# Kernel tuning notes

Measured on AMD Instinct MI355X. Metric: run time of the kernel, lower is better.

Reference implementation:

```python
import jax, jax.numpy as jnp
import numpy as np

N_NODES = 100_000
E_TOTAL = 1_100_000
# up_scale_edge_ranges: static metadata on the Data object -> baked as constants
EXCLUDE_RANGES = [(1_000_000, 1_100_000)]
_mask = np.ones(E_TOTAL, dtype=bool)
for _s, _e in EXCLUDE_RANGES:
    _mask[_s:_e] = False
KEEP_IDX = np.nonzero(_mask)[0]  # static, shape [1_000_000]


def _mlp(h, w1, b1, w2, b2):
    return jax.nn.relu(h @ w1 + b1) @ w2 + b2


def setup_inputs() -> dict:
    key = jax.random.key(0)
    ks = jax.random.split(key, 12)
    s = 0.05
    return {
        "x": jax.random.normal(ks[0], (N_NODES, 7), dtype=jnp.float32),
        "pos": jax.random.normal(ks[1], (N_NODES, 3), dtype=jnp.float32),
        "edge_index": jax.random.randint(ks[2], (2, E_TOTAL), 0, N_NODES, dtype=jnp.int64),
        "nw1": jax.random.normal(ks[3], (7, 128), dtype=jnp.float32) * s,
        "nb1": jnp.zeros((128,), dtype=jnp.float32),
        "nw2": jax.random.normal(ks[4], (128, 128), dtype=jnp.float32) * s,
        "nb2": jnp.zeros((128,), dtype=jnp.float32),
        "ew1": jax.random.normal(ks[5], (3, 128), dtype=jnp.float32) * s,
        "eb1": jnp.zeros((128,), dtype=jnp.float32),
        "ew2": jax.random.normal(ks[6], (128, 128), dtype=jnp.float32) * s,
        "eb2": jnp.zeros((128,), dtype=jnp.float32),
    }


def reference(x, pos, edge_index, nw1, nb1, nw2, nb2, ew1, eb1, ew2, eb2):
    # static mask over edge ranges (shapes fixed at trace time)
    edges = edge_index[:, KEEP_IDX]                       # [2, E_kept]
    d = pos[edges[0], :2] - pos[edges[1], :2]             # [E_kept, 2]
    norm = jnp.linalg.norm(d, axis=1, keepdims=True)      # [E_kept, 1]
    edges_attr = jnp.concatenate([d, norm], axis=1)       # [E_kept, 3]
    edge_embedding = _mlp(edges_attr, ew1, eb1, ew2, eb2) # [E_kept, 128]
    node_embedding = _mlp(x, nw1, nb1, nw2, nb2)          # [N, 128]
    return (node_embedding, edge_embedding)
```

## Files before the change

kernel.cpp:

```cpp
#include <hip/hip_runtime.h>

typedef short short8 __attribute__((ext_vector_type(8)));
typedef float f32x4 __attribute__((ext_vector_type(4)));
typedef unsigned int u32x2 __attribute__((ext_vector_type(2)));
typedef unsigned int u32x4 __attribute__((ext_vector_type(4)));

#define N_NODES   100000
#define E_KEEP    1000000
#define E_TOTAL_N 1100000
#define EDGE_OUT_BASE 12800000L

#define H1_STRIDE 272
#define STG_STRIDE 272

__device__ __forceinline__ unsigned short f2bf(float f) {
  unsigned int u = __builtin_bit_cast(unsigned int, f);
  u += 0x7fffu + ((u >> 16) & 1u);
  return (unsigned short)(u >> 16);
}

__device__ __forceinline__ unsigned int cvtpk(float lo, float hi) {
  unsigned int r;
  asm("v_cvt_pk_bf16_f32 %0, %1, %2" : "=v"(r) : "v"(lo), "v"(hi));
  return r;
}
__device__ __forceinline__ unsigned int pack2relu(float lo, float hi) {
  return cvtpk(fmaxf(lo, 0.f), fmaxf(hi, 0.f));
}
__device__ __forceinline__ unsigned int pack2(float lo, float hi) {
  return cvtpk(lo, hi);
}

__global__ void transpose_w2(const float* __restrict__ nw2,
                             const float* __restrict__ ew2,
                             unsigned short* __restrict__ ws) {
  int idx = blockIdx.x * 256 + threadIdx.x;
  for (int i = idx; i < 32768; i += 8192) {
    int m = i >> 14;
    int w = i & 16383;
    int k = w >> 7;
    int n = w & 127;
    const float* src = m ? ew2 : nw2;
    ws[m * 16384 + n * 128 + k] = f2bf(src[w]);
  }
}

struct SmemLayout {
  float w1f[7 * 128];
  float b1f[128];
  float b2f[128];
  float attr[256 * 7];
  char  h1[2][32 * H1_STRIDE];
  char  stg[32 * STG_STRIDE];
};

template<bool IS_EDGE>
__device__ __forceinline__ void run_path(
    const float* __restrict__ src,
    const int* __restrict__ ei,
    const float* __restrict__ w1,
    const float* __restrict__ b1,
    const float* __restrict__ b2,
    const unsigned short* __restrict__ w2t,
    float* __restrict__ outp, long out_base, int row_limit,
    int bid, SmemLayout& sm)
{
  constexpr int NA = IS_EDGE ? 3 : 7;
  const int t = threadIdx.x;

  if (t < 128) { sm.b1f[t] = b1[t]; sm.b2f[t] = b2[t]; }
  if (!IS_EDGE) {
    for (int i = t; i < 7 * 128; i += 256) sm.w1f[i] = w1[i];
  }

  {
    int r  = bid * 256 + t;
    int rl = r < row_limit ? r : row_limit - 1;
    if (IS_EDGE) {
      int si = ei[rl];
      int di = ei[E_TOTAL_N + rl];
      float ax = src[si * 3]     - src[di * 3];
      float ay = src[si * 3 + 1] - src[di * 3 + 1];
      sm.attr[t * 3 + 0] = ax;
      sm.attr[t * 3 + 1] = ay;
      sm.attr[t * 3 + 2] = sqrtf(ax * ax + ay * ay);
    } else {
#pragma unroll
      for (int cc = 0; cc < 7; ++cc) sm.attr[t * 7 + cc] = src[rl * 7 + cc];
    }
  }

  const int lane = t & 63;
  const int wid  = t >> 6;
  const int rg   = wid & 1;
  const int wc   = wid >> 1;
  const int c    = lane & 15;
  const int g    = lane >> 4;

  short8 wfrag[4][4];
#pragma unroll
  for (int nf = 0; nf < 4; ++nf)
#pragma unroll
    for (int kk = 0; kk < 4; ++kk)
      wfrag[nf][kk] = *(const short8*)(w2t + (wc * 64 + nf * 16 + c) * 128 + kk * 32 + g * 8);

  const int brow = t & 31;
  const int kc   = t >> 5;
  const int k0   = kc * 16;

  f32x4 w1r[IS_EDGE ? 12 : 1];
  if (IS_EDGE) {
#pragma unroll
    for (int cc = 0; cc < 3; ++cc)
#pragma unroll
      for (int q = 0; q < 4; ++q)
        w1r[cc * 4 + q] = *(const f32x4*)&w1[cc * 128 + k0 + q * 4];
  }

  const int rrow = rg * 16 + c;

  __syncthreads();

  for (int s = 0; s < 8; ++s) {
    char* h1 = sm.h1[s & 1];

    {
      float a[NA];
#pragma unroll
      for (int cc = 0; cc < NA; ++cc) a[cc] = sm.attr[(s * 32 + brow) * NA + cc];

      f32x4 h0 = *(const f32x4*)&sm.b1f[k0];
      f32x4 h1v = *(const f32x4*)&sm.b1f[k0 + 4];
      f32x4 h2 = *(const f32x4*)&sm.b1f[k0 + 8];
      f32x4 h3 = *(const f32x4*)&sm.b1f[k0 + 12];
      if (IS_EDGE) {
#pragma unroll
        for (int cc = 0; cc < 3; ++cc) {
          h0  += a[cc] * w1r[cc * 4 + 0];
          h1v += a[cc] * w1r[cc * 4 + 1];
          h2  += a[cc] * w1r[cc * 4 + 2];
          h3  += a[cc] * w1r[cc * 4 + 3];
        }
      } else {
#pragma unroll
        for (int cc = 0; cc < NA; ++cc) {
          h0  += a[cc] * *(const f32x4*)&sm.w1f[cc * 128 + k0];
          h1v += a[cc] * *(const f32x4*)&sm.w1f[cc * 128 + k0 + 4];
          h2  += a[cc] * *(const f32x4*)&sm.w1f[cc * 128 + k0 + 8];
          h3  += a[cc] * *(const f32x4*)&sm.w1f[cc * 128 + k0 + 12];
        }
      }
      u32x4 dA, dB;
      dA[0] = pack2relu(h0[0], h0[1]);  dA[1] = pack2relu(h0[2], h0[3]);
      dA[2] = pack2relu(h1v[0], h1v[1]); dA[3] = pack2relu(h1v[2], h1v[3]);
      dB[0] = pack2relu(h2[0], h2[1]);  dB[1] = pack2relu(h2[2], h2[3]);
      dB[2] = pack2relu(h3[0], h3[1]);  dB[3] = pack2relu(h3[2], h3[3]);

      char* wp = h1 + brow * H1_STRIDE + kc * 32;
      *(u32x4*)(wp)      = dA;
      *(u32x4*)(wp + 16) = dB;
    }

    __syncthreads();

    {
      f32x4 acc0 = {}, acc1 = {}, acc2 = {}, acc3 = {};
#pragma unroll
      for (int kk = 0; kk < 4; ++kk) {
        short8 hf = *(const short8*)(h1 + rrow * H1_STRIDE + kk * 64 + g * 16);
        acc0 = __builtin_amdgcn_mfma_f32_16x16x32_bf16(wfrag[0][kk], hf, acc0, 0, 0, 0);
        acc1 = __builtin_amdgcn_mfma_f32_16x16x32_bf16(wfrag[1][kk], hf, acc1, 0, 0, 0);
        acc2 = __builtin_amdgcn_mfma_f32_16x16x32_bf16(wfrag[2][kk], hf, acc2, 0, 0, 0);
        acc3 = __builtin_amdgcn_mfma_f32_16x16x32_bf16(wfrag[3][kk], hf, acc3, 0, 0, 0);
      }
      char* wp = sm.stg + rrow * STG_STRIDE + (wc * 64 + g * 4) * 2;
      f32x4 av[4] = {acc0, acc1, acc2, acc3};
#pragma unroll
      for (int nf = 0; nf < 4; ++nf) {
        f32x4 bv = *(const f32x4*)&sm.b2f[wc * 64 + nf * 16 + g * 4];
        f32x4 o = av[nf] + bv;
        u32x2 d;
        d[0] = pack2(o[0], o[1]);
        d[1] = pack2(o[2], o[3]);
        *(u32x2*)(wp + nf * 32) = d;
      }
    }

    __syncthreads();

    {
      int r0 = bid * 256 + s * 32;
#pragma unroll
      for (int p = 0; p < 2; ++p) {
        int u   = p * 256 + t;
        int row = u >> 4;
        int k16 = u & 15;
        if (r0 + row < row_limit) {
          short8 v = *(const short8*)(sm.stg + row * STG_STRIDE + k16 * 16);
          f32x4 lo, hi;
#pragma unroll
          for (int j = 0; j < 4; ++j) {
            lo[j] = __builtin_bit_cast(float, ((unsigned int)(unsigned short)v[j]) << 16);
            hi[j] = __builtin_bit_cast(float, ((unsigned int)(unsigned short)v[4 + j]) << 16);
          }
          float* op = outp + out_base + (long)(r0 + row) * 128 + k16 * 8;
          *(f32x4*)op       = lo;
          *(f32x4*)(op + 4) = hi;
        }
      }
    }
  }
}

__global__ __launch_bounds__(256, 3) void encoder_kernel(
    const float* __restrict__ x,
    const float* __restrict__ pos,
    const int* __restrict__ ei,
    const float* __restrict__ nw1,
    const float* __restrict__ nb1,
    const float* __restrict__ nb2,
    const float* __restrict__ ew1,
    const float* __restrict__ eb1,
    const float* __restrict__ eb2,
    const unsigned short* __restrict__ ws,
    float* __restrict__ outp,
    int nodeBlocks)
{
  __shared__ SmemLayout sm;
  int bid = blockIdx.x;
  if (bid < nodeBlocks) {
    run_path<false>(x, nullptr, nw1, nb1, nb2, ws, outp, 0L, N_NODES, bid, sm);
  } else {
    run_path<true>(pos, ei, ew1, eb1, eb2, ws + 16384, outp, EDGE_OUT_BASE,
                   E_KEEP, bid - nodeBlocks, sm);
  }
}

extern "C" void kernel_launch(void* const* d_in, const int* in_sizes, int n_in,
                              void* d_out, int out_size, void* d_ws, size_t ws_size,
                              hipStream_t stream) {
  const float* x   = (const float*)d_in[0];
  const float* pos = (const float*)d_in[1];
  const int*   ei  = (const int*)d_in[2];
  const float* nw1 = (const float*)d_in[3];
  const float* nb1 = (const float*)d_in[4];
  const float* nw2 = (const float*)d_in[5];
  const float* nb2 = (const float*)d_in[6];
  const float* ew1 = (const float*)d_in[7];
  const float* eb1 = (const float*)d_in[8];
  const float* ew2 = (const float*)d_in[9];
  const float* eb2 = (const float*)d_in[10];
  unsigned short* ws   = (unsigned short*)d_ws;
  float*          outp = (float*)d_out;

  transpose_w2<<<32, 256, 0, stream>>>(nw2, ew2, ws);

  int nodeBlocks = (N_NODES + 255) / 256;
  int edgeBlocks = (E_KEEP + 255) / 256;
  encoder_kernel<<<nodeBlocks + edgeBlocks, 256, 0, stream>>>(
      x, pos, ei, nw1, nb1, nb2, ew1, eb1, eb2, ws, outp, nodeBlocks);
}
```

Measured before the change: 163.0 us.

## Use nontemporal output stores, XCD-aware block remap, padded edge attrs, hoisted bias

Output stores become nontemporal so the large fp32 embedding writes bypass cache retention. Block IDs are remapped so each XCD handles a contiguous range of blocks, giving better L2 locality. Edge attributes are padded to stride 4 so they can be written and read with single vector LDS accesses, and the second-layer bias is loaded into registers once instead of every iteration. The register hoist adds pressure under launch bounds of 3 blocks per SM, and the remap changes the order in which blocks are scheduled.

```diff
diff --git a/kernel.cpp b/kernel.cpp
--- a/kernel.cpp
+++ b/kernel.cpp
@@ -26,9 +26,6 @@
 }
 __device__ __forceinline__ unsigned int pack2relu(float lo, float hi) {
   return cvtpk(fmaxf(lo, 0.f), fmaxf(hi, 0.f));
-}
-__device__ __forceinline__ unsigned int pack2(float lo, float hi) {
-  return cvtpk(lo, hi);
 }
 
 __global__ void transpose_w2(const float* __restrict__ nw2,
@@ -66,6 +63,7 @@
     int bid, SmemLayout& sm)
 {
   constexpr int NA = IS_EDGE ? 3 : 7;
+  constexpr int ASTRIDE = IS_EDGE ? 4 : 7;
   const int t = threadIdx.x;
 
   if (t < 128) { sm.b1f[t] = b1[t]; sm.b2f[t] = b2[t]; }
@@ -81,9 +79,8 @@
       int di = ei[E_TOTAL_N + rl];
       float ax = src[si * 3]     - src[di * 3];
       float ay = src[si * 3 + 1] - src[di * 3 + 1];
-      sm.attr[t * 3 + 0] = ax;
-      sm.attr[t * 3 + 1] = ay;
-      sm.attr[t * 3 + 2] = sqrtf(ax * ax + ay * ay);
+      f32x4 a4 = {ax, ay, sqrtf(ax * ax + ay * ay), 0.f};
+      *(f32x4*)&sm.attr[t * 4] = a4;
     } else {
 #pragma unroll
       for (int cc = 0; cc < 7; ++cc) sm.attr[t * 7 + cc] = src[rl * 7 + cc];
@@ -121,13 +118,24 @@
 
   __syncthreads();
 
+  f32x4 b2v[4];
+#pragma unroll
+  for (int nf = 0; nf < 4; ++nf)
+    b2v[nf] = *(const f32x4*)&sm.b2f[wc * 64 + nf * 16 + g * 4];
+
   for (int s = 0; s < 8; ++s) {
     char* h1 = sm.h1[s & 1];
 
     {
       float a[NA];
-#pragma unroll
-      for (int cc = 0; cc < NA; ++cc) a[cc] = sm.attr[(s * 32 + brow) * NA + cc];
+      if (IS_EDGE) {
+        f32x4 a4 = *(const f32x4*)&sm.attr[(s * 32 + brow) * 4];
+        a[0] = a4[0]; a[1] = a4[1]; a[2] = a4[2];
+      } else {
+#pragma unroll
+        for (int cc = 0; cc < NA; ++cc)
+          a[cc] = sm.attr[(s * 32 + brow) * ASTRIDE + cc];
+      }
 
       f32x4 h0 = *(const f32x4*)&sm.b1f[k0];
       f32x4 h1v = *(const f32x4*)&sm.b1f[k0 + 4];
@@ -174,14 +182,12 @@
         acc3 = __builtin_amdgcn_mfma_f32_16x16x32_bf16(wfrag[3][kk], hf, acc3, 0, 0, 0);
       }
       char* wp = sm.stg + rrow * STG_STRIDE + (wc * 64 + g * 4) * 2;
-      f32x4 av[4] = {acc0, acc1, acc2, acc3};
+      f32x4 av[4] = {acc0 + b2v[0], acc1 + b2v[1], acc2 + b2v[2], acc3 + b2v[3]};
 #pragma unroll
       for (int nf = 0; nf < 4; ++nf) {
-        f32x4 bv = *(const f32x4*)&sm.b2f[wc * 64 + nf * 16 + g * 4];
-        f32x4 o = av[nf] + bv;
         u32x2 d;
-        d[0] = pack2(o[0], o[1]);
-        d[1] = pack2(o[2], o[3]);
+        d[0] = cvtpk(av[nf][0], av[nf][1]);
+        d[1] = cvtpk(av[nf][2], av[nf][3]);
         *(u32x2*)(wp + nf * 32) = d;
       }
     }
@@ -204,8 +210,8 @@
             hi[j] = __builtin_bit_cast(float, ((unsigned int)(unsigned short)v[4 + j]) << 16);
           }
           float* op = outp + out_base + (long)(r0 + row) * 128 + k16 * 8;
-          *(f32x4*)op       = lo;
-          *(f32x4*)(op + 4) = hi;
+          __builtin_nontemporal_store(lo, (f32x4*)op);
+          __builtin_nontemporal_store(hi, (f32x4*)(op + 4));
         }
       }
     }
@@ -224,10 +230,14 @@
     const float* __restrict__ eb2,
     const unsigned short* __restrict__ ws,
     float* __restrict__ outp,
-    int nodeBlocks)
+    int nodeBlocks, int totalBlocks)
 {
   __shared__ SmemLayout sm;
-  int bid = blockIdx.x;
+  int orig = blockIdx.x;
+  int q = totalBlocks >> 3, r = totalBlocks & 7;
+  int xcd = orig & 7, idx = orig >> 3;
+  int bid = (xcd < r ? xcd * (q + 1) : r * (q + 1) + (xcd - r) * q) + idx;
+
   if (bid < nodeBlocks) {
     run_path<false>(x, nullptr, nw1, nb1, nb2, ws, outp, 0L, N_NODES, bid, sm);
   } else {
@@ -257,6 +267,7 @@
 
   int nodeBlocks = (N_NODES + 255) / 256;
   int edgeBlocks = (E_KEEP + 255) / 256;
-  encoder_kernel<<<nodeBlocks + edgeBlocks, 256, 0, stream>>>(
-      x, pos, ei, nw1, nb1, nb2, ew1, eb1, eb2, ws, outp, nodeBlocks);
-}
+  int totalBlocks = nodeBlocks + edgeBlocks;
+  encoder_kernel<<<totalBlocks, 256, 0, stream>>>(
+      x, pos, ei, nw1, nb1, nb2, ew1, eb1, eb2, ws, outp, nodeBlocks, totalBlocks);
+}
```

New measurement: 241.8 us. 1.48x slower.
